# Performance work log

Measured on AMD Instinct MI355X. Metric: run time of the kernel, lower is better.

The kernel has to match this reference:

```python
import jax, jax.numpy as jnp
import numpy as np

T, I, H = 4096, 2048, 2048


def setup_inputs() -> dict:
    key = jax.random.key(0)
    ks = jax.random.split(key, 7)
    s = 0.075
    return {
        "x": jax.random.normal(ks[0], (1, T, I), dtype=jnp.float32),
        "W_ih": jax.random.normal(ks[1], (4 * H, I), dtype=jnp.float32) * s,
        "W_hh": jax.random.normal(ks[2], (4 * H, H), dtype=jnp.float32) * s,
        "b_ih": jax.random.normal(ks[3], (4 * H,), dtype=jnp.float32) * s,
        "b_hh": jax.random.normal(ks[4], (4 * H,), dtype=jnp.float32) * s,
        "Wo": jax.random.normal(ks[5], (I, H), dtype=jnp.float32) * s,
        "bo": jax.random.normal(ks[6], (I,), dtype=jnp.float32) * s,
    }


def reference(x, W_ih, W_hh, b_ih, b_hh, Wo, bo):
    xs = x[0]  # [T, I]  (batch dim of 1 squeezed, as in original)
    # Precompute input projections for all timesteps in one big GEMM: [T, 4H]
    gx = xs @ W_ih.T + (b_ih + b_hh)

    def step(carry, gxt):
        h, c = carry  # [H], [H]
        g = gxt + W_hh @ h  # [4H]; PyTorch gate order: i, f, g, o
        i_g, f_g, g_g, o_g = jnp.split(g, 4)
        c_new = jax.nn.sigmoid(f_g) * c + jax.nn.sigmoid(i_g) * jnp.tanh(g_g)
        h_new = jax.nn.sigmoid(o_g) * jnp.tanh(c_new)
        return (h_new, c_new), h_new

    h0 = jnp.zeros((H,), dtype=x.dtype)
    c0 = jnp.zeros((H,), dtype=x.dtype)
    _, hs = jax.lax.scan(step, (h0, c0), gx)  # hs: [T, H]

    out = jax.nn.sigmoid(hs @ Wo.T + bo)  # [T, I]
    return out[None]  # [1, T, I]
```

## Files before the change

### kernel.cpp

```cpp
#include <hip/hip_runtime.h>

#define T_STEPS 4096
#define IDIM 2048
#define HDIM 2048
#define G4DIM 8192

typedef __attribute__((ext_vector_type(8))) short short8;
typedef __attribute__((ext_vector_type(4))) float f32x4;
typedef __attribute__((ext_vector_type(2))) float f32x2;

__device__ __forceinline__ unsigned short f2bf(float f) {
  unsigned int u = __float_as_uint(f);
  u += 0x7fffu + ((u >> 16) & 1u);
  return (unsigned short)(u >> 16);
}
__device__ __forceinline__ float bf2f(unsigned short h) {
  return __uint_as_float(((unsigned int)h) << 16);
}

template <int ACT_SIGMOID, int OUT_BF16>
__global__ __launch_bounds__(256) void gemm_bt(
    const float* __restrict__ A, const float* __restrict__ B,
    const float* __restrict__ bias, void* __restrict__ Cout,
    int M, int N, int K)
{
  __shared__ short Ah[64][40];
  __shared__ short Al[64][40];
  __shared__ short Bh[64][40];
  __shared__ short Bl[64][40];
  const int tid  = threadIdx.x;
  const int wave = tid >> 6, lane = tid & 63;
  const int bn = blockIdx.x * 64, bm = blockIdx.y * 64;
  const int srow = tid >> 2, sc8 = (tid & 3) * 8;
  const int wm = (wave >> 1) * 32, wn = (wave & 1) * 32;
  const int lq = lane >> 4, lr = lane & 15;
  f32x4 acc[2][2] = {};

  for (int k0 = 0; k0 < K; k0 += 32) {
    __syncthreads();
    {
      const float* src = A + (size_t)(bm + srow) * K + k0 + sc8;
      float4 v0 = *(const float4*)(src);
      float4 v1 = *(const float4*)(src + 4);
      float vv[8] = {v0.x, v0.y, v0.z, v0.w, v1.x, v1.y, v1.z, v1.w};
      short8 vh, vl;
      #pragma unroll
      for (int i = 0; i < 8; ++i) {
        unsigned short hb = f2bf(vv[i]);
        vh[i] = (short)hb;
        vl[i] = (short)f2bf(vv[i] - bf2f(hb));
      }
      *(short8*)&Ah[srow][sc8] = vh;
      *(short8*)&Al[srow][sc8] = vl;
    }
    {
      const float* src = B + (size_t)(bn + srow) * K + k0 + sc8;
      float4 v0 = *(const float4*)(src);
      float4 v1 = *(const float4*)(src + 4);
      float vv[8] = {v0.x, v0.y, v0.z, v0.w, v1.x, v1.y, v1.z, v1.w};
      short8 vh, vl;
      #pragma unroll
      for (int i = 0; i < 8; ++i) {
        unsigned short hb = f2bf(vv[i]);
        vh[i] = (short)hb;
        vl[i] = (short)f2bf(vv[i] - bf2f(hb));
      }
      *(short8*)&Bh[srow][sc8] = vh;
      *(short8*)&Bl[srow][sc8] = vl;
    }
    __syncthreads();

    short8 ah0 = *(const short8*)&Ah[wm +      lr][lq * 8];
    short8 al0 = *(const short8*)&Al[wm +      lr][lq * 8];
    short8 ah1 = *(const short8*)&Ah[wm + 16 + lr][lq * 8];
    short8 al1 = *(const short8*)&Al[wm + 16 + lr][lq * 8];
    short8 bh0 = *(const short8*)&Bh[wn +      lr][lq * 8];
    short8 bl0 = *(const short8*)&Bl[wn +      lr][lq * 8];
    short8 bh1 = *(const short8*)&Bh[wn + 16 + lr][lq * 8];
    short8 bl1 = *(const short8*)&Bl[wn + 16 + lr][lq * 8];

    acc[0][0] = __builtin_amdgcn_mfma_f32_16x16x32_bf16(ah0, bh0, acc[0][0], 0, 0, 0);
    acc[0][0] = __builtin_amdgcn_mfma_f32_16x16x32_bf16(ah0, bl0, acc[0][0], 0, 0, 0);
    acc[0][0] = __builtin_amdgcn_mfma_f32_16x16x32_bf16(al0, bh0, acc[0][0], 0, 0, 0);

    acc[0][1] = __builtin_amdgcn_mfma_f32_16x16x32_bf16(ah0, bh1, acc[0][1], 0, 0, 0);
    acc[0][1] = __builtin_amdgcn_mfma_f32_16x16x32_bf16(ah0, bl1, acc[0][1], 0, 0, 0);
    acc[0][1] = __builtin_amdgcn_mfma_f32_16x16x32_bf16(al0, bh1, acc[0][1], 0, 0, 0);

    acc[1][0] = __builtin_amdgcn_mfma_f32_16x16x32_bf16(ah1, bh0, acc[1][0], 0, 0, 0);
    acc[1][0] = __builtin_amdgcn_mfma_f32_16x16x32_bf16(ah1, bl0, acc[1][0], 0, 0, 0);
    acc[1][0] = __builtin_amdgcn_mfma_f32_16x16x32_bf16(al1, bh0, acc[1][0], 0, 0, 0);

    acc[1][1] = __builtin_amdgcn_mfma_f32_16x16x32_bf16(ah1, bh1, acc[1][1], 0, 0, 0);
    acc[1][1] = __builtin_amdgcn_mfma_f32_16x16x32_bf16(ah1, bl1, acc[1][1], 0, 0, 0);
    acc[1][1] = __builtin_amdgcn_mfma_f32_16x16x32_bf16(al1, bh1, acc[1][1], 0, 0, 0);
  }

  #pragma unroll
  for (int mi = 0; mi < 2; ++mi) {
    #pragma unroll
    for (int ni = 0; ni < 2; ++ni) {
      #pragma unroll
      for (int rr = 0; rr < 4; ++rr) {
        int row = bm + wm + mi * 16 + lq * 4 + rr;
        int col = bn + wn + ni * 16 + lr;
        float v = acc[mi][ni][rr];
        if (bias) v += bias[col];
        if (ACT_SIGMOID) v = 1.f / (1.f + __expf(-v));
        if (OUT_BF16)
          ((unsigned short*)Cout)[(size_t)row * N + col] = f2bf(v);
        else
          ((float*)Cout)[(size_t)row * N + col] = v;
      }
    }
  }
}

__global__ __launch_bounds__(1024, 4) void lstm_scan(
    const float* __restrict__ Whh,
    const float* __restrict__ b_ih, const float* __restrict__ b_hh,
    const unsigned short* __restrict__ gx,
    float* __restrict__ hs)
{
  const int b   = blockIdx.x;
  const int tid = threadIdx.x;
  const int u   = tid & 7;
  const int kc  = tid >> 3;
  const int wv  = tid >> 6;
  const int lane = tid & 63;

  f32x2 w2[4][8];
  #pragma unroll
  for (int g = 0; g < 4; ++g) {
    const float* wp = Whh + (size_t)(g * HDIM + b * 8 + u) * HDIM + kc * 16;
    #pragma unroll
    for (int i = 0; i < 4; ++i) {
      float4 v = *(const float4*)(wp + 4 * i);
      w2[g][2 * i]     = f32x2{v.x, v.y};
      w2[g][2 * i + 1] = f32x2{v.z, v.w};
    }
  }
  float bias_r = 0.f;
  if (tid < 32) {
    int br = (tid >> 3) * HDIM + b * 8 + (tid & 7);
    bias_r = b_ih[br] + b_hh[br];
  }
  float cval = 0.f;

  __shared__ float h_lds[128 * 20];
  __shared__ float partials[2][32][17];
  __shared__ int   seqs[2][16];
  if (tid < 32) ((int*)seqs)[tid] = -1;
  __syncthreads();

  unsigned int* hs_u = (unsigned int*)hs;

  const unsigned short* gxp = gx + (tid >> 3) * HDIM + b * 8 + (tid & 7);
  unsigned short gxr_cur = 0, gxr_nxt = 0;
  if (tid < 32) gxr_cur = gxp[0];

  for (int t = 0; t < T_STEPS; ++t) {
    const int buf = t & 1;
    if (tid < 32 && t + 1 < T_STEPS)
      gxr_nxt = gxp[(size_t)(t + 1) * G4DIM];

    f32x2 h2w;
    if (t > 0) {
      const unsigned long long* p =
          (const unsigned long long*)(hs_u + (size_t)(t - 1) * HDIM + tid * 2);
      unsigned long long a =
          __hip_atomic_load(p, __ATOMIC_RELAXED, __HIP_MEMORY_SCOPE_AGENT);
      for (;;) {
        unsigned long long nb =
            __hip_atomic_load(p, __ATOMIC_RELAXED, __HIP_MEMORY_SCOPE_AGENT);
        unsigned int lo = (unsigned int)a, hi = (unsigned int)(a >> 32);
        if (lo != 0xAAAAAAAAu && hi != 0xAAAAAAAAu) {
          h2w = f32x2{__uint_as_float(lo), __uint_as_float(hi)};
          break;
        }
        __builtin_amdgcn_s_sleep(1);
        a = nb;
      }
    } else {
      h2w = f32x2{0.f, 0.f};
    }

    *(f32x2*)&h_lds[kc * 20 + u * 2] = h2w;

    f32x2 acc0{0.f, 0.f}, acc1{0.f, 0.f}, acc2{0.f, 0.f}, acc3{0.f, 0.f};
    #pragma unroll
    for (int i = 0; i < 4; ++i) {
      float4 hv = *(const float4*)&h_lds[kc * 20 + i * 4];
      f32x2 ha{hv.x, hv.y}, hb{hv.z, hv.w};
      acc0 += w2[0][2 * i] * ha;  acc0 += w2[0][2 * i + 1] * hb;
      acc1 += w2[1][2 * i] * ha;  acc1 += w2[1][2 * i + 1] * hb;
      acc2 += w2[2][2 * i] * ha;  acc2 += w2[2][2 * i + 1] * hb;
      acc3 += w2[3][2 * i] * ha;  acc3 += w2[3][2 * i + 1] * hb;
    }
    float s0 = acc0[0] + acc0[1];
    float s1 = acc1[0] + acc1[1];
    float s2 = acc2[0] + acc2[1];
    float s3 = acc3[0] + acc3[1];
    #pragma unroll
    for (int m = 8; m <= 32; m <<= 1) {
      s0 += __shfl_xor(s0, m, 64);
      s1 += __shfl_xor(s1, m, 64);
      s2 += __shfl_xor(s2, m, 64);
      s3 += __shfl_xor(s3, m, 64);
    }
    if ((tid & 56) == 0) {
      partials[buf][0 * 8 + u][wv] = s0;
      partials[buf][1 * 8 + u][wv] = s1;
      partials[buf][2 * 8 + u][wv] = s2;
      partials[buf][3 * 8 + u][wv] = s3;
    }
    if (lane == 0)
      __hip_atomic_store(&seqs[buf][wv], t, __ATOMIC_RELEASE,
                         __HIP_MEMORY_SCOPE_WORKGROUP);

    if (tid < 64) {
      const int sidx = lane & 15;
      for (;;) {
        int sv = __hip_atomic_load(&seqs[buf][sidx], __ATOMIC_ACQUIRE,
                                   __HIP_MEMORY_SCOPE_WORKGROUP);
        if (__all(sv >= t)) break;
      }
      __builtin_amdgcn_s_setprio(1);
      float gval = 0.f;
      if (tid < 32) {
        float s = bf2f(gxr_cur) + bias_r;
        const float* pr = &partials[buf][tid][0];
        #pragma unroll
        for (int i = 0; i < 4; ++i) {
          float4 v = *(const float4*)(pr + 4 * i);
          s += (v.x + v.y) + (v.z + v.w);
        }
        gval = s;
      }
      float g_i = __shfl(gval, tid);
      float g_f = __shfl(gval, tid + 8);
      float g_g = __shfl(gval, tid + 16);
      float g_o = __shfl(gval, tid + 24);
      if (tid < 8) {
        float is = 1.f / (1.f + __expf(-g_i));
        float fs = 1.f / (1.f + __expf(-g_f));
        float os = 1.f / (1.f + __expf(-g_o));
        float e2 = __expf(-2.f * fabsf(g_g));
        float tg = (1.f - e2) / (1.f + e2);
        tg = (g_g < 0.f) ? -tg : tg;
        float cn = fs * cval + is * tg;
        cval = cn;
        float ec = __expf(-2.f * fabsf(cn));
        float tc = (1.f - ec) / (1.f + ec);
        tc = (cn < 0.f) ? -tc : tc;
        float hn = os * tc;
        __hip_atomic_store(hs_u + (size_t)t * HDIM + b * 8 + tid,
                           __float_as_uint(hn),
                           __ATOMIC_RELAXED, __HIP_MEMORY_SCOPE_AGENT);
      }
      __builtin_amdgcn_s_setprio(0);
    }
    gxr_cur = gxr_nxt;
  }
}

extern "C" void kernel_launch(void* const* d_in, const int* in_sizes, int n_in,
                              void* d_out, int out_size, void* d_ws, size_t ws_size,
                              hipStream_t stream) {
  (void)in_sizes; (void)n_in; (void)out_size; (void)ws_size;
  const float* x    = (const float*)d_in[0];
  const float* W_ih = (const float*)d_in[1];
  const float* W_hh = (const float*)d_in[2];
  const float* b_ih = (const float*)d_in[3];
  const float* b_hh = (const float*)d_in[4];
  const float* Wo   = (const float*)d_in[5];
  const float* bo   = (const float*)d_in[6];
  float* out = (float*)d_out;

  char* ws = (char*)d_ws;
  unsigned short* gx = (unsigned short*)ws;
  float* hs = (float*)(ws + (size_t)T_STEPS * G4DIM * 2);

  hipMemsetAsync(hs, 0xAA, (size_t)T_STEPS * HDIM * sizeof(float), stream);

  gemm_bt<0, 1><<<dim3(G4DIM / 64, T_STEPS / 64), 256, 0, stream>>>(
      x, W_ih, nullptr, gx, T_STEPS, G4DIM, IDIM);

  lstm_scan<<<256, 1024, 0, stream>>>(W_hh, b_ih, b_hh, gx, hs);

  gemm_bt<1, 0><<<dim3(IDIM / 64, T_STEPS / 64), 256, 0, stream>>>(
      hs, Wo, bo, out, T_STEPS, IDIM, HDIM);
}
```

Measured before the change: 12.87 ms.

## Fuse output projection into LSTM scan and replace seq-flag sync with barrier

```diff
diff --git a/kernel.cpp b/kernel.cpp
--- a/kernel.cpp
+++ b/kernel.cpp
@@ -120,13 +120,16 @@
     const float* __restrict__ Whh,
     const float* __restrict__ b_ih, const float* __restrict__ b_hh,
     const unsigned short* __restrict__ gx,
-    float* __restrict__ hs)
+    float* __restrict__ hs,
+    const float* __restrict__ Wo,
+    const float* __restrict__ bo,
+    float* __restrict__ out)
 {
-  const int b   = blockIdx.x;
-  const int tid = threadIdx.x;
-  const int u   = tid & 7;
-  const int kc  = tid >> 3;
-  const int wv  = tid >> 6;
+  const int b    = blockIdx.x;
+  const int tid  = threadIdx.x;
+  const int u    = tid & 7;
+  const int kc   = tid >> 3;
+  const int wv   = tid >> 6;
   const int lane = tid & 63;
 
   f32x2 w2[4][8];
@@ -140,91 +143,97 @@
       w2[g][2 * i + 1] = f32x2{v.z, v.w};
     }
   }
+  f32x2 wo2[8];
+  {
+    const float* wop = Wo + (size_t)(b * 8 + u) * HDIM + kc * 16;
+    #pragma unroll
+    for (int i = 0; i < 4; ++i) {
+      float4 v = *(const float4*)(wop + 4 * i);
+      wo2[2 * i]     = f32x2{v.x, v.y};
+      wo2[2 * i + 1] = f32x2{v.z, v.w};
+    }
+  }
   float bias_r = 0.f;
   if (tid < 32) {
     int br = (tid >> 3) * HDIM + b * 8 + (tid & 7);
     bias_r = b_ih[br] + b_hh[br];
   }
+  float bo_r = 0.f;
+  if (wv == 1 && lane < 8) bo_r = bo[b * 8 + lane];
   float cval = 0.f;
 
   __shared__ float h_lds[128 * 20];
   __shared__ float partials[2][32][17];
-  __shared__ int   seqs[2][16];
-  if (tid < 32) ((int*)seqs)[tid] = -1;
-  __syncthreads();
-
+  __shared__ float opart[2][8][17];
   unsigned int* hs_u = (unsigned int*)hs;
 
   const unsigned short* gxp = gx + (tid >> 3) * HDIM + b * 8 + (tid & 7);
   unsigned short gxr_cur = 0, gxr_nxt = 0;
   if (tid < 32) gxr_cur = gxp[0];
 
-  for (int t = 0; t < T_STEPS; ++t) {
-    const int buf = t & 1;
+  for (int t = 0; t < T_STEPS + 2; ++t) {
+    const int  buf      = t & 1;
+    const bool do_gates = (t < T_STEPS);
+    const bool do_hload = (t >= 1 && t <= T_STEPS);
     if (tid < 32 && t + 1 < T_STEPS)
       gxr_nxt = gxp[(size_t)(t + 1) * G4DIM];
 
-    f32x2 h2w;
-    if (t > 0) {
+    if (do_hload) {
       const unsigned long long* p =
           (const unsigned long long*)(hs_u + (size_t)(t - 1) * HDIM + tid * 2);
-      unsigned long long a =
-          __hip_atomic_load(p, __ATOMIC_RELAXED, __HIP_MEMORY_SCOPE_AGENT);
+      #define PLOAD() __hip_atomic_load(p, __ATOMIC_RELAXED, __HIP_MEMORY_SCOPE_AGENT)
+      #define POK(x) (((unsigned int)(x) != 0xAAAAAAAAu) && \
+                      ((unsigned int)((x) >> 32) != 0xAAAAAAAAu))
+      unsigned long long r0 = PLOAD(), r1 = PLOAD(), r2 = PLOAD(), r3 = PLOAD();
+      unsigned long long v;
       for (;;) {
-        unsigned long long nb =
-            __hip_atomic_load(p, __ATOMIC_RELAXED, __HIP_MEMORY_SCOPE_AGENT);
-        unsigned int lo = (unsigned int)a, hi = (unsigned int)(a >> 32);
-        if (lo != 0xAAAAAAAAu && hi != 0xAAAAAAAAu) {
-          h2w = f32x2{__uint_as_float(lo), __uint_as_float(hi)};
-          break;
-        }
-        __builtin_amdgcn_s_sleep(1);
-        a = nb;
-      }
-    } else {
-      h2w = f32x2{0.f, 0.f};
-    }
-
-    *(f32x2*)&h_lds[kc * 20 + u * 2] = h2w;
-
-    f32x2 acc0{0.f, 0.f}, acc1{0.f, 0.f}, acc2{0.f, 0.f}, acc3{0.f, 0.f};
-    #pragma unroll
-    for (int i = 0; i < 4; ++i) {
-      float4 hv = *(const float4*)&h_lds[kc * 20 + i * 4];
-      f32x2 ha{hv.x, hv.y}, hb{hv.z, hv.w};
-      acc0 += w2[0][2 * i] * ha;  acc0 += w2[0][2 * i + 1] * hb;
-      acc1 += w2[1][2 * i] * ha;  acc1 += w2[1][2 * i + 1] * hb;
-      acc2 += w2[2][2 * i] * ha;  acc2 += w2[2][2 * i + 1] * hb;
-      acc3 += w2[3][2 * i] * ha;  acc3 += w2[3][2 * i + 1] * hb;
-    }
-    float s0 = acc0[0] + acc0[1];
-    float s1 = acc1[0] + acc1[1];
-    float s2 = acc2[0] + acc2[1];
-    float s3 = acc3[0] + acc3[1];
-    #pragma unroll
-    for (int m = 8; m <= 32; m <<= 1) {
-      s0 += __shfl_xor(s0, m, 64);
-      s1 += __shfl_xor(s1, m, 64);
-      s2 += __shfl_xor(s2, m, 64);
-      s3 += __shfl_xor(s3, m, 64);
-    }
-    if ((tid & 56) == 0) {
-      partials[buf][0 * 8 + u][wv] = s0;
-      partials[buf][1 * 8 + u][wv] = s1;
-      partials[buf][2 * 8 + u][wv] = s2;
-      partials[buf][3 * 8 + u][wv] = s3;
-    }
-    if (lane == 0)
-      __hip_atomic_store(&seqs[buf][wv], t, __ATOMIC_RELEASE,
-                         __HIP_MEMORY_SCOPE_WORKGROUP);
-
-    if (tid < 64) {
-      const int sidx = lane & 15;
-      for (;;) {
-        int sv = __hip_atomic_load(&seqs[buf][sidx], __ATOMIC_ACQUIRE,
-                                   __HIP_MEMORY_SCOPE_WORKGROUP);
-        if (__all(sv >= t)) break;
-      }
+        if (POK(r0)) { v = r0; break; }  r0 = PLOAD();
+        if (POK(r1)) { v = r1; break; }  r1 = PLOAD();
+        if (POK(r2)) { v = r2; break; }  r2 = PLOAD();
+        if (POK(r3)) { v = r3; break; }  r3 = PLOAD();
+      }
+      #undef PLOAD
+      #undef POK
+      f32x2 h2w{__uint_as_float((unsigned int)v),
+                __uint_as_float((unsigned int)(v >> 32))};
+      *(f32x2*)&h_lds[kc * 20 + u * 2] = h2w;
+    } else if (t == 0) {
+      *(f32x2*)&h_lds[kc * 20 + u * 2] = f32x2{0.f, 0.f};
+    }
+
+    if (do_gates) {
+      f32x2 acc0{0.f, 0.f}, acc1{0.f, 0.f}, acc2{0.f, 0.f}, acc3{0.f, 0.f};
+      #pragma unroll
+      for (int i = 0; i < 4; ++i) {
+        float4 hv = *(const float4*)&h_lds[kc * 20 + i * 4];
+        f32x2 ha{hv.x, hv.y}, hb{hv.z, hv.w};
+        acc0 += w2[0][2 * i] * ha;  acc0 += w2[0][2 * i + 1] * hb;
+        acc1 += w2[1][2 * i] * ha;  acc1 += w2[1][2 * i + 1] * hb;
+        acc2 += w2[2][2 * i] * ha;  acc2 += w2[2][2 * i + 1] * hb;
+        acc3 += w2[3][2 * i] * ha;  acc3 += w2[3][2 * i + 1] * hb;
+      }
+      float s0 = acc0[0] + acc0[1];
+      float s1 = acc1[0] + acc1[1];
+      float s2 = acc2[0] + acc2[1];
+      float s3 = acc3[0] + acc3[1];
+      #pragma unroll
+      for (int m = 8; m <= 32; m <<= 1) {
+        s0 += __shfl_xor(s0, m, 64);
+        s1 += __shfl_xor(s1, m, 64);
+        s2 += __shfl_xor(s2, m, 64);
+        s3 += __shfl_xor(s3, m, 64);
+      }
+      if ((tid & 56) == 0) {
+        partials[buf][0 * 8 + u][wv] = s0;
+        partials[buf][1 * 8 + u][wv] = s1;
+        partials[buf][2 * 8 + u][wv] = s2;
+        partials[buf][3 * 8 + u][wv] = s3;
+      }
+    }
+
+    __syncthreads();
+
+    if (do_gates && tid < 64) {
       __builtin_amdgcn_s_setprio(1);
       float gval = 0.f;
       if (tid < 32) {
@@ -260,6 +269,33 @@
       }
       __builtin_amdgcn_s_setprio(0);
     }
+
+    if (do_hload) {
+      f32x2 oa{0.f, 0.f};
+      #pragma unroll
+      for (int i = 0; i < 4; ++i) {
+        float4 hv = *(const float4*)&h_lds[kc * 20 + i * 4];
+        oa += wo2[2 * i]     * f32x2{hv.x, hv.y};
+        oa += wo2[2 * i + 1] * f32x2{hv.z, hv.w};
+      }
+      float so = oa[0] + oa[1];
+      #pragma unroll
+      for (int m = 8; m <= 32; m <<= 1) so += __shfl_xor(so, m, 64);
+      if ((tid & 56) == 0) opart[buf][u][wv] = so;
+    }
+
+    if (wv == 1 && lane < 8 && t >= 2) {
+      float s = bo_r;
+      const float* pr = &opart[(t - 1) & 1][lane][0];
+      #pragma unroll
+      for (int i = 0; i < 4; ++i) {
+        float4 v = *(const float4*)(pr + 4 * i);
+        s += (v.x + v.y) + (v.z + v.w);
+      }
+      s = 1.f / (1.f + __expf(-s));
+      out[(size_t)(t - 2) * IDIM + b * 8 + lane] = s;
+    }
+
     gxr_cur = gxr_nxt;
   }
 }
@@ -286,8 +322,5 @@
   gemm_bt<0, 1><<<dim3(G4DIM / 64, T_STEPS / 64), 256, 0, stream>>>(
       x, W_ih, nullptr, gx, T_STEPS, G4DIM, IDIM);
 
-  lstm_scan<<<256, 1024, 0, stream>>>(W_hh, b_ih, b_hh, gx, hs);
-
-  gemm_bt<1, 0><<<dim3(IDIM / 64, T_STEPS / 64), 256, 0, stream>>>(
-      hs, Wo, bo, out, T_STEPS, IDIM, HDIM);
-}
+  lstm_scan<<<256, 1024, 0, stream>>>(W_hh, b_ih, b_hh, gx, hs, Wo, bo, out);
+}
```

Result: slower. 14.76 ms (+14.7%).
